# Kernel optimization log

Measured on AMD Instinct MI355X. Metric: run time of the kernel, lower is better.

Reference implementation:

```python
import jax, jax.numpy as jnp
import numpy as np

B, M, N = 4, 1024, 4096
DQ, DC, H, DH = 512, 512, 8, 64
D = H * DH
NEG = -10000000.0


def setup_inputs() -> dict:
    key = jax.random.key(0)
    ks = jax.random.split(key, 7)
    left = jax.random.normal(ks[0], (B, M, DQ), dtype=jnp.float32)
    right = jax.random.normal(ks[1], (B, N, DC), dtype=jnp.float32)
    mask = jax.random.randint(ks[2], (B, M, N), 0, 2).astype(bool)
    # learned params (torch Linear stores weight as (out,in); we store (in,out))
    Wq = jax.random.normal(ks[3], (DQ, D), dtype=jnp.float32) * (DQ ** -0.5)
    Wkv = jax.random.normal(ks[4], (DC, 2 * D), dtype=jnp.float32) * (DC ** -0.5)
    Wout = jax.random.normal(ks[5], (D, DQ), dtype=jnp.float32) * (D ** -0.5)
    bout = jax.random.normal(ks[6], (DQ,), dtype=jnp.float32) * 0.01
    return {"left": left, "right": right, "mask": mask,
            "Wq": Wq, "Wkv": Wkv, "Wout": Wout, "bout": bout}


def reference(left, right, mask, Wq, Wkv, Wout, bout):
    scale = DH ** -0.5
    q = left @ Wq                      # (B, M, D)
    kv = right @ Wkv                   # (B, N, 2D)
    k, v = jnp.split(kv, 2, axis=-1)   # (B, N, D) each
    q = q.reshape(B, M, H, DH).transpose(0, 2, 1, 3)  # (B, H, M, DH)
    k = k.reshape(B, N, H, DH).transpose(0, 2, 1, 3)  # (B, H, N, DH)
    v = v.reshape(B, N, H, DH).transpose(0, 2, 1, 3)  # (B, H, N, DH)
    sim = scale * jnp.einsum('bhmd,bhnd->bhmn', q, k)  # (B, H, M, N)
    sim = jnp.where(mask[:, None, :, :], sim, NEG)
    attn = jax.nn.softmax(sim, axis=-1)
    out = jnp.einsum('bhmn,bhnd->bhmd', attn, v)       # (B, H, M, DH)
    out = out.transpose(0, 2, 1, 3).reshape(B, M, D)
    return out @ Wout + bout           # (B, M, DQ)
```

## Files before the change

kernel.cpp:

```cpp
#include <hip/hip_runtime.h>

typedef _Float16 f16;
typedef __attribute__((ext_vector_type(8))) _Float16 half8;
typedef __attribute__((ext_vector_type(4))) _Float16 half4;
typedef __attribute__((ext_vector_type(4))) float floatx4;
typedef unsigned int uint32;

#define MFMA16(a, b, c) __builtin_amdgcn_mfma_f32_16x16x32_f16((a), (b), (c), 0, 0, 0)

constexpr int B_ = 4, M_ = 1024, N_ = 4096, DQ_ = 512, DC_ = 512, H_ = 8, DH_ = 64, D_ = 512;
constexpr int KP_ = 576;
constexpr int VP_ = 4224;
constexpr int NSPLIT = 4;
constexpr float SCL_ = 0.125f * 1.44269504089f;

typedef __attribute__((address_space(1))) const void glds_g;
typedef __attribute__((address_space(3))) void glds_l;
__device__ __forceinline__ void g2lds16(const void* g, void* l) {
    __builtin_amdgcn_global_load_lds((glds_g*)g, (glds_l*)l, 16, 0, 0);
}

__device__ __forceinline__ void wtr_tile(const float* __restrict__ src, f16* __restrict__ dst,
                                         int Nout, int bx, int by, int tid) {
    __shared__ __align__(16) f16 Ts[64][72];
    const int n0 = bx * 64, k0 = by * 64;
    {
        int kr = tid >> 2, q4 = tid & 3;
        const float* sp = src + (size_t)(k0 + kr) * Nout + n0 + q4 * 16;
        float4 x0 = *(const float4*)(sp + 0), x1 = *(const float4*)(sp + 4);
        float4 x2 = *(const float4*)(sp + 8), x3 = *(const float4*)(sp + 12);
        half8 h0, h1;
        h0[0]=(f16)x0.x; h0[1]=(f16)x0.y; h0[2]=(f16)x0.z; h0[3]=(f16)x0.w;
        h0[4]=(f16)x1.x; h0[5]=(f16)x1.y; h0[6]=(f16)x1.z; h0[7]=(f16)x1.w;
        h1[0]=(f16)x2.x; h1[1]=(f16)x2.y; h1[2]=(f16)x2.z; h1[3]=(f16)x2.w;
        h1[4]=(f16)x3.x; h1[5]=(f16)x3.y; h1[6]=(f16)x3.z; h1[7]=(f16)x3.w;
        *(half8*)&Ts[kr][q4 * 16] = h0;
        *(half8*)&Ts[kr][q4 * 16 + 8] = h1;
    }
    __syncthreads();
    {
        int nr = tid >> 2, q = tid & 3;
        half8 h0, h1;
#pragma unroll
        for (int j = 0; j < 8; j++) { h0[j] = Ts[q * 16 + j][nr]; h1[j] = Ts[q * 16 + 8 + j][nr]; }
        f16* dp = dst + (size_t)(n0 + nr) * 512 + k0 + q * 16;
        *(half8*)(dp + 0) = h0;
        *(half8*)(dp + 8) = h1;
    }
}

__global__ __launch_bounds__(256)
void prep_k(const void* __restrict__ mask, uint32* __restrict__ bits,
            const float* __restrict__ left, f16* __restrict__ leftb,
            const float* __restrict__ right, f16* __restrict__ rightb,
            const float* __restrict__ Wq, f16* __restrict__ wqt,
            const float* __restrict__ Wkv, f16* __restrict__ wkvt,
            const float* __restrict__ Wout, f16* __restrict__ woutt) {
    const int blk = blockIdx.x, tid = threadIdx.x;
    if (blk < 4096) {
        __shared__ int s_bad;
        if (tid == 0) s_bad = 0;
        __syncthreads();
        const uint32* w = (const uint32*)mask;
        int bad = 0;
#pragma unroll
        for (int j = 0; j < 4; j++) bad |= (w[tid * 4 + j] & 0xFFFFFFFEu) != 0u;
        if (bad) s_bad = 1;
        __syncthreads();
        const bool bytes_mode = s_bad != 0;
        const size_t base = (size_t)blk * 4096;
        const int lane = tid & 63;
        for (int j = 0; j < 16; j++) {
            size_t e = base + j * 256 + tid;
            bool pred = bytes_mode ? (((const unsigned char*)mask)[e] != 0)
                                   : (((const int*)mask)[e] != 0);
            unsigned long long bal = __ballot(pred);
            if (lane == 0)       bits[e >> 5] = (uint32)bal;
            else if (lane == 32) bits[e >> 5] = (uint32)(bal >> 32);
        }
    } else if (blk < 6144) {
        int i = ((blk - 4096) * 256 + tid) * 4;
        float4 x = *(const float4*)(left + i);
        half4 h; h[0] = (f16)x.x; h[1] = (f16)x.y; h[2] = (f16)x.z; h[3] = (f16)x.w;
        *(half4*)(leftb + i) = h;
    } else if (blk < 14336) {
        int i = ((blk - 6144) * 256 + tid) * 4;
        float4 x = *(const float4*)(right + i);
        half4 h; h[0] = (f16)x.x; h[1] = (f16)x.y; h[2] = (f16)x.z; h[3] = (f16)x.w;
        *(half4*)(rightb + i) = h;
    } else if (blk < 14400) {
        int r = blk - 14336;
        wtr_tile(Wq, wqt, 512, r & 7, r >> 3, tid);
    } else if (blk < 14528) {
        int r = blk - 14400;
        wtr_tile(Wkv, wkvt, 1024, r & 15, r >> 4, tid);
    } else {
        int r = blk - 14528;
        wtr_tile(Wout, woutt, 512, r & 7, r >> 3, tid);
    }
}

__global__ __launch_bounds__(256)
void gemmqkv_k(const f16* __restrict__ leftb, const f16* __restrict__ wqt,
               const f16* __restrict__ rightb, const f16* __restrict__ wkvt,
               f16* __restrict__ qb, f16* __restrict__ kb, f16* __restrict__ vt) {
    __shared__ __align__(16) f16 As[128 * 32];
    __shared__ __align__(16) f16 Bs[128 * 32];
    const int blk = blockIdx.x, tid = threadIdx.x;
    const int lane = tid & 63, wave = tid >> 6;
    const int qd = lane >> 4, l16 = lane & 15;
    const int wm = wave >> 1, wn = wave & 1;

    const bool iskv = blk < 1024;
    const f16* A; const f16* Bt; size_t m0, n0;
    if (iskv) { A = rightb; Bt = wkvt; m0 = (size_t)(blk >> 3) * 128; n0 = (size_t)(blk & 7) * 128; }
    else      { int r = blk - 1024; A = leftb; Bt = wqt; m0 = (size_t)(r >> 2) * 128; n0 = (size_t)(r & 3) * 128; }

    const int c1 = wave * 64 + lane;
    const int c2 = 256 + c1;
    f16* la1 = As + (size_t)(wave * 64) * 8;
    f16* la2 = As + (size_t)(256 + wave * 64) * 8;
    f16* lb1 = Bs + (size_t)(wave * 64) * 8;
    f16* lb2 = Bs + (size_t)(256 + wave * 64) * 8;

    floatx4 acc[4][4] = {};

    for (int k0 = 0; k0 < 512; k0 += 32) {
        __syncthreads();
        g2lds16(A + (m0 + (c1 >> 2)) * 512 + k0 + (c1 & 3) * 8, la1);
        g2lds16(A + (m0 + (c2 >> 2)) * 512 + k0 + (c2 & 3) * 8, la2);
        g2lds16(Bt + (n0 + (c1 >> 2)) * 512 + k0 + (c1 & 3) * 8, lb1);
        g2lds16(Bt + (n0 + (c2 >> 2)) * 512 + k0 + (c2 & 3) * 8, lb2);
        __syncthreads();
        half8 a[4], b[4];
#pragma unroll
        for (int t = 0; t < 4; t++) {
            a[t] = *(const half8*)&As[(wm * 64 + t * 16 + l16) * 32 + qd * 8];
            b[t] = *(const half8*)&Bs[(wn * 64 + t * 16 + l16) * 32 + qd * 8];
        }
#pragma unroll
        for (int mt = 0; mt < 4; mt++)
#pragma unroll
            for (int nt = 0; nt < 4; nt++)
                acc[mt][nt] = MFMA16(a[mt], b[nt], acc[mt][nt]);
    }

#pragma unroll
    for (int mt = 0; mt < 4; mt++)
#pragma unroll
        for (int nt = 0; nt < 4; nt++)
#pragma unroll
            for (int r = 0; r < 4; r++) {
                size_t row = m0 + wm * 64 + mt * 16 + qd * 4 + r;
                size_t col = n0 + wn * 64 + nt * 16 + l16;
                float v = acc[mt][nt][r];
                if (!iskv) {
                    qb[row * 512 + col] = (f16)v;
                } else if (col < 512) {
                    kb[row * KP_ + col] = (f16)v;
                } else {
                    int dcol = (int)col - 512;
                    int hh = dcol >> 6, dh = dcol & 63;
                    size_t bb = row >> 12, nn = row & 4095;
                    vt[((bb * H_ + hh) * (size_t)DH_ + dh) * VP_ + nn] = (f16)v;
                }
            }
}

__global__ __launch_bounds__(256)
void attn_k(const f16* __restrict__ Qb, const f16* __restrict__ Kb,
            const f16* __restrict__ Vt, const uint32* __restrict__ mb,
            float* __restrict__ Op, float* __restrict__ Lp) {
    const int tid = threadIdx.x;
    const int lane = tid & 63, wave = tid >> 6;
    const int qd = lane >> 4, l16 = lane & 15;
    const int bh = blockIdx.y, b = bh >> 3, h = bh & 7;
    const int z = blockIdx.z;
    constexpr int iters = N_ / (64 * NSPLIT);
    const int n_base = z * iters * 64;
    const int m_base = blockIdx.x * 128 + wave * 32;

    __shared__ __align__(16) f16 Ks[64][72];
    __shared__ __align__(16) f16 Vs[64][72];
    __shared__ __align__(16) f16 psh[4][32][72];

    const f16 scl = (f16)SCL_;
    half8 q[2][2];
#pragma unroll
    for (int f = 0; f < 2; f++) {
        const f16* qrow = Qb + ((size_t)(b * M_ + m_base + f * 16 + l16)) * D_ + h * DH_;
        q[f][0] = *(const half8*)(qrow + qd * 8);
        q[f][1] = *(const half8*)(qrow + 32 + qd * 8);
#pragma unroll
        for (int j = 0; j < 8; j++) { q[f][0][j] = q[f][0][j] * scl; q[f][1][j] = q[f][1][j] * scl; }
    }
    const half8 ONE = {(f16)1, (f16)1, (f16)1, (f16)1, (f16)1, (f16)1, (f16)1, (f16)1};

    floatx4 o[2][4] = {};
    floatx4 ol[2] = {};
    const uint32* mbase = mb + ((size_t)(b * M_ + m_base)) * (N_ / 32);

    const int snr = tid >> 2, scc = tid & 3;
    const f16* kg = Kb + ((size_t)(b * N_) + snr) * KP_ + h * DH_ + scc * 8;
    const f16* vg = Vt + ((size_t)bh * DH_ + snr) * VP_ + scc * 8;

    for (int it = 0; it < iters; it++) {
        const int n0 = n_base + it * 64;
        half8 kc0 = *(const half8*)(kg + (size_t)n0 * KP_);
        half8 kc1 = *(const half8*)(kg + (size_t)n0 * KP_ + 32);
        half8 vc0 = *(const half8*)(vg + n0);
        half8 vc1 = *(const half8*)(vg + n0 + 32);
        __syncthreads();
        *(half8*)&Ks[snr][scc * 8]      = kc0;
        *(half8*)&Ks[snr][32 + scc * 8] = kc1;
        *(half8*)&Vs[snr][scc * 8]      = vc0;
        *(half8*)&Vs[snr][32 + scc * 8] = vc1;
        __syncthreads();

        const int wi = n0 >> 5;
        uint32 wm[2][4][2];
#pragma unroll
        for (int f = 0; f < 2; f++)
#pragma unroll
            for (int r = 0; r < 4; r++) {
                const uint32* mr = mbase + (size_t)(f * 16 + qd * 4 + r) * (N_ / 32);
                uint2 mm = *(const uint2*)(mr + wi);
                wm[f][r][0] = mm.x;
                wm[f][r][1] = mm.y;
            }

#pragma unroll
        for (int s = 0; s < 4; s++) {
            half8 k0 = *(const half8*)&Ks[s * 16 + l16][qd * 8];
            half8 k1 = *(const half8*)&Ks[s * 16 + l16][32 + qd * 8];
#pragma unroll
            for (int f = 0; f < 2; f++) {
                floatx4 t = {};
                t = MFMA16(q[f][0], k0, t);
                t = MFMA16(q[f][1], k1, t);
#pragma unroll
                for (int r = 0; r < 4; r++) {
                    uint32 w = (s < 2) ? wm[f][r][0] : wm[f][r][1];
                    int sh = (s * 16 + l16) & 31;
                    float e = exp2f(t[r]);
                    e = ((w >> sh) & 1u) ? e : 0.0f;
                    psh[wave][f * 16 + qd * 4 + r][s * 16 + l16] = (f16)e;
                }
            }
        }
        half8 pa[2][2];
#pragma unroll
        for (int f = 0; f < 2; f++) {
            pa[f][0] = *(const half8*)&psh[wave][f * 16 + l16][qd * 8];
            pa[f][1] = *(const half8*)&psh[wave][f * 16 + l16][32 + qd * 8];
        }
#pragma unroll
        for (int f = 0; f < 2; f++) {
            ol[f] = MFMA16(pa[f][0], ONE, ol[f]);
            ol[f] = MFMA16(pa[f][1], ONE, ol[f]);
        }
#pragma unroll
        for (int s = 0; s < 4; s++) {
            half8 v0 = *(const half8*)&Vs[s * 16 + l16][qd * 8];
            half8 v1 = *(const half8*)&Vs[s * 16 + l16][32 + qd * 8];
#pragma unroll
            for (int f = 0; f < 2; f++) {
                o[f][s] = MFMA16(pa[f][0], v0, o[f][s]);
                o[f][s] = MFMA16(pa[f][1], v1, o[f][s]);
            }
        }
    }

#pragma unroll
    for (int f = 0; f < 2; f++)
#pragma unroll
        for (int r = 0; r < 4; r++) {
            size_t row = (size_t)(z * 32 + bh) * M_ + m_base + f * 16 + qd * 4 + r;
            float* op = Op + row * DH_;
#pragma unroll
            for (int s = 0; s < 4; s++) op[s * 16 + l16] = o[f][s][r];
            if (l16 == 0) Lp[row] = ol[f][r];
        }
}

__global__ __launch_bounds__(256)
void comb_k(const float* __restrict__ Op, const float* __restrict__ Lp, f16* __restrict__ Ob) {
    int i = blockIdx.x * 256 + threadIdx.x;
    int d = i & 63, m = (i >> 6) & 1023, bh = i >> 16;
    float num = 0.f, den = 0.f;
#pragma unroll
    for (int s = 0; s < NSPLIT; s++) {
        size_t row = ((size_t)s * 32 + bh) * M_ + m;
        num += Op[row * DH_ + d];
        den += Lp[row];
    }
    int b = bh >> 3, h = bh & 7;
    Ob[((size_t)(b * M_ + m)) * D_ + h * DH_ + d] = (f16)(num / den);
}

__global__ __launch_bounds__(256)
void gemmout_k(const f16* __restrict__ A, const f16* __restrict__ Bt,
               float* __restrict__ Fout, const float* __restrict__ bias) {
    __shared__ __align__(16) f16 As[128 * 32];
    __shared__ __align__(16) f16 Bs[128 * 32];
    const int tid = threadIdx.x;
    const int lane = tid & 63, wave = tid >> 6;
    const int qd = lane >> 4, l16 = lane & 15;
    const int wm = wave >> 1, wn = wave & 1;
    const size_t m0 = (size_t)blockIdx.x * 128;
    const size_t n0 = (size_t)blockIdx.y * 128;

    const int c1 = wave * 64 + lane;
    const int c2 = 256 + c1;
    f16* la1 = As + (size_t)(wave * 64) * 8;
    f16* la2 = As + (size_t)(256 + wave * 64) * 8;
    f16* lb1 = Bs + (size_t)(wave * 64) * 8;
    f16* lb2 = Bs + (size_t)(256 + wave * 64) * 8;

    floatx4 acc[4][4] = {};

    for (int k0 = 0; k0 < 512; k0 += 32) {
        __syncthreads();
        g2lds16(A + (m0 + (c1 >> 2)) * 512 + k0 + (c1 & 3) * 8, la1);
        g2lds16(A + (m0 + (c2 >> 2)) * 512 + k0 + (c2 & 3) * 8, la2);
        g2lds16(Bt + (n0 + (c1 >> 2)) * 512 + k0 + (c1 & 3) * 8, lb1);
        g2lds16(Bt + (n0 + (c2 >> 2)) * 512 + k0 + (c2 & 3) * 8, lb2);
        __syncthreads();
        half8 a[4], b[4];
#pragma unroll
        for (int t = 0; t < 4; t++) {
            a[t] = *(const half8*)&As[(wm * 64 + t * 16 + l16) * 32 + qd * 8];
            b[t] = *(const half8*)&Bs[(wn * 64 + t * 16 + l16) * 32 + qd * 8];
        }
#pragma unroll
        for (int mt = 0; mt < 4; mt++)
#pragma unroll
            for (int nt = 0; nt < 4; nt++)
                acc[mt][nt] = MFMA16(a[mt], b[nt], acc[mt][nt]);
    }

#pragma unroll
    for (int mt = 0; mt < 4; mt++)
#pragma unroll
        for (int nt = 0; nt < 4; nt++)
#pragma unroll
            for (int r = 0; r < 4; r++) {
                size_t row = m0 + wm * 64 + mt * 16 + qd * 4 + r;
                size_t col = n0 + wn * 64 + nt * 16 + l16;
                Fout[row * 512 + col] = acc[mt][nt][r] + bias[col];
            }
}

extern "C" void kernel_launch(void* const* d_in, const int* in_sizes, int n_in,
                              void* d_out, int out_size, void* d_ws, size_t ws_size,
                              hipStream_t stream) {
    const float* left  = (const float*)d_in[0];
    const float* right = (const float*)d_in[1];
    const void*  mask  = d_in[2];
    const float* Wq    = (const float*)d_in[3];
    const float* Wkv   = (const float*)d_in[4];
    const float* Wout  = (const float*)d_in[5];
    const float* bout  = (const float*)d_in[6];

    char* ws = (char*)d_ws;
    size_t off = 0;
    auto take = [&](size_t bytes) { char* p = ws + off; off += (bytes + 255) & ~(size_t)255; return p; };
    uint32* mbits = (uint32*)take((size_t)B_ * M_ * N_ / 8);
    f16* woutt = (f16*)take((size_t)D_ * DQ_ * 2);
    f16* qb    = (f16*)take((size_t)B_ * M_ * D_ * 2);
    f16* kb    = (f16*)take((size_t)B_ * N_ * KP_ * 2);
    f16* vt    = (f16*)take((size_t)B_ * H_ * DH_ * VP_ * 2);
    f16* ob    = (f16*)take((size_t)B_ * M_ * D_ * 2);
    char* pool = (char*)take((size_t)34 * 1024 * 1024);
    f16* leftb  = (f16*)pool;
    f16* rightb = (f16*)(pool + (size_t)4 * 1024 * 1024);
    f16* wqt    = (f16*)(pool + (size_t)20 * 1024 * 1024);
    f16* wkvt   = (f16*)(pool + (size_t)21 * 1024 * 1024);
    float* Op   = (float*)pool;
    float* Lp   = (float*)(pool + (size_t)NSPLIT * 32 * M_ * DH_ * 4);

    prep_k<<<14592, 256, 0, stream>>>(mask, mbits, left, leftb, right, rightb,
                                      Wq, wqt, Wkv, wkvt, Wout, woutt);
    gemmqkv_k<<<1152, 256, 0, stream>>>(leftb, wqt, rightb, wkvt, qb, kb, vt);
    attn_k<<<dim3(8, 32, NSPLIT), 256, 0, stream>>>(qb, kb, vt, mbits, Op, Lp);
    comb_k<<<8192, 256, 0, stream>>>(Op, Lp, ob);
    gemmout_k<<<dim3(32, 4), 256, 0, stream>>>(ob, woutt, (float*)d_out, bout);
}
```

Before: 304.4 us.

## Transpose V-projection GEMM and PV MFMA for coalesced stores; simplify mask bits

The V half of the KV projection now runs as a transposed GEMM (Wkv^T times right^T). Its tile outputs then land contiguously along the sequence dimension of the transposed V buffer, instead of as strided scattered stores. In attention, the PV and row-sum MFMAs swap operands so each lane holds a contiguous output row, and partial results are written as floatx4 vectors. Mask words are pre-shifted per lane, and exp2f with a folded log2e is replaced by __expf with a plain scale. The mask-format check in prep_k now reads a per-block chunk rather than always the first chunk, which also changes correctness behaviour.

Result: faster. 283.2 us (-6.9%).

```diff
diff --git a/kernel.cpp b/kernel.cpp
--- a/kernel.cpp
+++ b/kernel.cpp
@@ -12,7 +12,7 @@
 constexpr int KP_ = 576;
 constexpr int VP_ = 4224;
 constexpr int NSPLIT = 4;
-constexpr float SCL_ = 0.125f * 1.44269504089f;
+constexpr float SCL_ = 0.125f;
 
 typedef __attribute__((address_space(1))) const void glds_g;
 typedef __attribute__((address_space(3))) void glds_l;
@@ -61,7 +61,7 @@
         __shared__ int s_bad;
         if (tid == 0) s_bad = 0;
         __syncthreads();
-        const uint32* w = (const uint32*)mask;
+        const uint32* w = (const uint32*)mask + (size_t)blk * 1024;
         int bad = 0;
 #pragma unroll
         for (int j = 0; j < 4; j++) bad |= (w[tid * 4 + j] & 0xFFFFFFFEu) != 0u;
@@ -111,10 +111,17 @@
     const int qd = lane >> 4, l16 = lane & 15;
     const int wm = wave >> 1, wn = wave & 1;
 
-    const bool iskv = blk < 1024;
+    int mode;
     const f16* A; const f16* Bt; size_t m0, n0;
-    if (iskv) { A = rightb; Bt = wkvt; m0 = (size_t)(blk >> 3) * 128; n0 = (size_t)(blk & 7) * 128; }
-    else      { int r = blk - 1024; A = leftb; Bt = wqt; m0 = (size_t)(r >> 2) * 128; n0 = (size_t)(r & 3) * 128; }
+    if (blk < 1024) {
+        size_t rows = (size_t)(blk >> 3) * 128, cols = (size_t)(blk & 7) * 128;
+        if (cols < 512) { mode = 0; A = rightb; m0 = rows; Bt = wkvt;   n0 = cols; }
+        else            { mode = 1; A = wkvt;   m0 = cols; Bt = rightb; n0 = rows; }
+    } else {
+        int r = blk - 1024;
+        mode = 2; A = leftb; Bt = wqt;
+        m0 = (size_t)(r >> 2) * 128; n0 = (size_t)(r & 3) * 128;
+    }
 
     const int c1 = wave * 64 + lane;
     const int c2 = 256 + c1;
@@ -151,17 +158,17 @@
         for (int nt = 0; nt < 4; nt++)
 #pragma unroll
             for (int r = 0; r < 4; r++) {
-                size_t row = m0 + wm * 64 + mt * 16 + qd * 4 + r;
-                size_t col = n0 + wn * 64 + nt * 16 + l16;
+                size_t mi = m0 + wm * 64 + mt * 16 + qd * 4 + r;
+                size_t ni = n0 + wn * 64 + nt * 16 + l16;
                 float v = acc[mt][nt][r];
-                if (!iskv) {
-                    qb[row * 512 + col] = (f16)v;
-                } else if (col < 512) {
-                    kb[row * KP_ + col] = (f16)v;
+                if (mode == 2) {
+                    qb[mi * 512 + ni] = (f16)v;
+                } else if (mode == 0) {
+                    kb[mi * KP_ + ni] = (f16)v;
                 } else {
-                    int dcol = (int)col - 512;
+                    int dcol = (int)mi - 512;
                     int hh = dcol >> 6, dh = dcol & 63;
-                    size_t bb = row >> 12, nn = row & 4095;
+                    size_t bb = ni >> 12, nn = ni & 4095;
                     vt[((bb * H_ + hh) * (size_t)DH_ + dh) * VP_ + nn] = (f16)v;
                 }
             }
@@ -196,7 +203,7 @@
     }
     const half8 ONE = {(f16)1, (f16)1, (f16)1, (f16)1, (f16)1, (f16)1, (f16)1, (f16)1};
 
-    floatx4 o[2][4] = {};
+    floatx4 ot[2][4] = {};
     floatx4 ol[2] = {};
     const uint32* mbase = mb + ((size_t)(b * M_ + m_base)) * (N_ / 32);
 
@@ -218,15 +225,15 @@
         __syncthreads();
 
         const int wi = n0 >> 5;
-        uint32 wm[2][4][2];
+        uint32 msk[2][4][2];
 #pragma unroll
         for (int f = 0; f < 2; f++)
 #pragma unroll
             for (int r = 0; r < 4; r++) {
                 const uint32* mr = mbase + (size_t)(f * 16 + qd * 4 + r) * (N_ / 32);
                 uint2 mm = *(const uint2*)(mr + wi);
-                wm[f][r][0] = mm.x;
-                wm[f][r][1] = mm.y;
+                msk[f][r][0] = mm.x >> l16;
+                msk[f][r][1] = mm.y >> l16;
             }
 
 #pragma unroll
@@ -240,10 +247,9 @@
                 t = MFMA16(q[f][1], k1, t);
 #pragma unroll
                 for (int r = 0; r < 4; r++) {
-                    uint32 w = (s < 2) ? wm[f][r][0] : wm[f][r][1];
-                    int sh = (s * 16 + l16) & 31;
-                    float e = exp2f(t[r]);
-                    e = ((w >> sh) & 1u) ? e : 0.0f;
+                    uint32 bit = (msk[f][r][s >> 1] >> ((s & 1) * 16)) & 1u;
+                    float e = __expf(t[r]);
+                    e = bit ? e : 0.0f;
                     psh[wave][f * 16 + qd * 4 + r][s * 16 + l16] = (f16)e;
                 }
             }
@@ -256,31 +262,30 @@
         }
 #pragma unroll
         for (int f = 0; f < 2; f++) {
-            ol[f] = MFMA16(pa[f][0], ONE, ol[f]);
-            ol[f] = MFMA16(pa[f][1], ONE, ol[f]);
-        }
-#pragma unroll
-        for (int s = 0; s < 4; s++) {
-            half8 v0 = *(const half8*)&Vs[s * 16 + l16][qd * 8];
-            half8 v1 = *(const half8*)&Vs[s * 16 + l16][32 + qd * 8];
+            ol[f] = MFMA16(ONE, pa[f][0], ol[f]);
+            ol[f] = MFMA16(ONE, pa[f][1], ol[f]);
+        }
+#pragma unroll
+        for (int sd = 0; sd < 4; sd++) {
+            half8 v0 = *(const half8*)&Vs[sd * 16 + l16][qd * 8];
+            half8 v1 = *(const half8*)&Vs[sd * 16 + l16][32 + qd * 8];
 #pragma unroll
             for (int f = 0; f < 2; f++) {
-                o[f][s] = MFMA16(pa[f][0], v0, o[f][s]);
-                o[f][s] = MFMA16(pa[f][1], v1, o[f][s]);
-            }
-        }
-    }
-
-#pragma unroll
-    for (int f = 0; f < 2; f++)
-#pragma unroll
-        for (int r = 0; r < 4; r++) {
-            size_t row = (size_t)(z * 32 + bh) * M_ + m_base + f * 16 + qd * 4 + r;
-            float* op = Op + row * DH_;
-#pragma unroll
-            for (int s = 0; s < 4; s++) op[s * 16 + l16] = o[f][s][r];
-            if (l16 == 0) Lp[row] = ol[f][r];
-        }
+                ot[f][sd] = MFMA16(v0, pa[f][0], ot[f][sd]);
+                ot[f][sd] = MFMA16(v1, pa[f][1], ot[f][sd]);
+            }
+        }
+    }
+
+#pragma unroll
+    for (int f = 0; f < 2; f++) {
+        size_t row = (size_t)(z * 32 + bh) * M_ + m_base + f * 16 + l16;
+        float* op = Op + row * DH_ + qd * 4;
+#pragma unroll
+        for (int sd = 0; sd < 4; sd++)
+            *(floatx4*)(op + sd * 16) = ot[f][sd];
+        if (qd == 0) Lp[row] = ol[f][0];
+    }
 }
 
 __global__ __launch_bounds__(256)
```
